# Kernel tuning notes

Hardware: AMD Instinct MI355X
Metric: run time of the kernel (lower is better)

The kernel has to match this reference:

```python
import jax, jax.numpy as jnp
import numpy as np

B, N, D0 = 128, 128, 512   # batch, n_objects, obj_dim
H, KD, R = 32, 64, 16      # n_heads, key_dim, n_relations
D = D0 + 1                 # with temporal tag

def setup_inputs() -> dict:
    key = jax.random.key(0)
    k1, k2, k3, k4, k5 = jax.random.split(key, 5)
    s = 0.02
    return {
        'obj_seq': jax.random.normal(k1, (B, N, D0), jnp.float32),
        'W_k':  jax.random.normal(k2, (KD, D), jnp.float32) * s,
        'W_q1': jax.random.normal(k3, (H * KD, D * N), jnp.float32) * s,
        'W_q2': jax.random.normal(k4, (H * KD, D * N), jnp.float32) * s,
        'W_s':  jax.random.normal(k5, (R, D), jnp.float32) * s,
    }

def reference(obj_seq, W_k, W_q1, W_q2, W_s):
    b, n, _ = obj_seq.shape
    # append temporal tag channel: obj -> [B, N, D]
    tag = jnp.broadcast_to(jnp.arange(n, dtype=obj_seq.dtype)[None, :, None], (b, n, 1))
    obj = jnp.concatenate([obj_seq, tag], axis=2)
    flat = obj.reshape(b, -1)                      # [B, N*D]
    Q1 = (flat @ W_q1.T).reshape(b, H, KD)         # [B, H, KD]
    Q2 = (flat @ W_q2.T).reshape(b, H, KD)
    K = obj @ W_k.T                                # [B, N, KD]
    # scores [B, N, H], softmax over objects (dim=1 in torch)
    A1 = jax.nn.softmax(jnp.einsum('bhk,bnk->bnh', Q1, K), axis=1)
    A2 = jax.nn.softmax(jnp.einsum('bhk,bnk->bnh', Q2, K), axis=1)
    # attention-weighted object sums: [B, H, D]
    E1 = jnp.einsum('bnh,bnd->bhd', A1, obj)
    E2 = jnp.einsum('bnh,bnd->bhd', A2, obj)
    Dr = E1 @ W_s.T - E2 @ W_s.T                   # [B, H, R]
    Dr = jnp.concatenate([Dr, E1[:, :, -1:], E2[:, :, -1:]], axis=2)  # [B, H, R+2]
    return Dr.reshape(b, -1)                       # [B, H*(R+2)]
```

## Files before the change

kernel.cpp:

```cpp
#include <hip/hip_runtime.h>
#include <cstdint>

typedef _Float16 f16;
typedef _Float16 f16x8 __attribute__((ext_vector_type(8)));
typedef short s16x8 __attribute__((ext_vector_type(8)));
typedef unsigned u32x4 __attribute__((ext_vector_type(4)));
typedef float f32x4 __attribute__((ext_vector_type(4)));
typedef float floatx4 __attribute__((ext_vector_type(4)));

#define KTOT 65664
#define KSTEPS 2052
#define DP 544

__device__ __forceinline__ void gload_lds16(const void* g, void* l) {
  __builtin_amdgcn_global_load_lds(
      (const __attribute__((address_space(1))) void*)g,
      (__attribute__((address_space(3))) void*)l, 16, 0, 0);
}

__device__ __forceinline__ unsigned bfpack(float e0, float e1) {
  return (__float_as_uint(e0) >> 16) | (__float_as_uint(e1) & 0xffff0000u);
}
__device__ __forceinline__ float bfhi(float x) {
  return __uint_as_float(__float_as_uint(x) & 0xffff0000u);
}

__global__ void prep_flat(const float* __restrict__ obj_seq, char* __restrict__ flatA) {
  int o = blockIdx.x * 256 + threadIdx.x;
  int row = o & 127;
  int k8 = (o >> 7) & 3;
  int pl = (o >> 9) & 1;
  int kb = o >> 10;
  int k0 = kb * 32 + k8 * 8;
  unsigned w[4];
#pragma unroll
  for (int j = 0; j < 8; j += 2) {
    float v[2];
#pragma unroll
    for (int jj = 0; jj < 2; ++jj) {
      int k = k0 + j + jj;
      int n = k / 513;
      int d = k - n * 513;
      float x = (d < 512) ? obj_seq[(((size_t)(row << 7) + n) << 9) + d] : (float)n;
      if (pl) x = x - bfhi(x);
      v[jj] = x;
    }
    w[j >> 1] = bfpack(v[0], v[1]);
  }
  *(u32x4*)(flatA + (size_t)o * 16) = (u32x4){w[0], w[1], w[2], w[3]};
}

__global__ void prep_obj(const float* __restrict__ obj_seq, f16* __restrict__ objHi,
                         f16* __restrict__ objLo, f16* __restrict__ objT16) {
  __shared__ f16 tile[32][132];
  int b = blockIdx.x / 17, c = blockIdx.x - 17 * (blockIdx.x / 17);
  int t = threadIdx.x;
  if (c < 16) {
#pragma unroll
    for (int i = 0; i < 16; ++i) {
      int e = t + i * 256;
      int n = e >> 5, dd = e & 31;
      float v = obj_seq[(((size_t)(b << 7) + n) << 9) + (c << 5) + dd];
      f16 h = (f16)v;
      objHi[((size_t)((b << 7) + n)) * DP + (c << 5) + dd] = h;
      objLo[((size_t)((b << 7) + n)) * DP + (c << 5) + dd] = (f16)(v - (float)h);
      tile[dd][n] = h;
    }
    __syncthreads();
#pragma unroll
    for (int i = 0; i < 16; ++i) {
      int e = t + i * 256;
      int dd = e >> 7, n = e & 127;
      objT16[(((size_t)b * DP + (c << 5) + dd) << 7) + n] = tile[dd][n];
    }
  } else {
#pragma unroll
    for (int i = 0; i < 16; ++i) {
      int e = t + i * 256;
      int n = e >> 5, dd = e & 31;
      f16 h = (dd == 0) ? (f16)(float)n : (f16)0.f;
      objHi[((size_t)((b << 7) + n)) * DP + 512 + dd] = h;
      objLo[((size_t)((b << 7) + n)) * DP + 512 + dd] = (f16)0.f;
    }
#pragma unroll
    for (int i = 0; i < 16; ++i) {
      int e = t + i * 256;
      int dd = e >> 7, n = e & 127;
      objT16[(((size_t)b * DP + 512 + dd) << 7) + n] = (dd == 0) ? (f16)(float)n : (f16)0.f;
    }
  }
}

__global__ void prep_wk(const float* __restrict__ W_k, f16* __restrict__ WkHi,
                        f16* __restrict__ WkLo) {
  int o = blockIdx.x * 256 + threadIdx.x;
  int kd = o / DP, d = o - kd * DP;
  float v = (d < 513) ? W_k[kd * 513 + d] * 1024.f : 0.f;
  f16 h = (f16)v;
  WkHi[o] = h;
  WkLo[o] = (f16)(v - (float)h);
}

__global__ __launch_bounds__(512, 2) void qgemm(const char* __restrict__ flatA,
                                                const float* __restrict__ Wq1,
                                                const float* __restrict__ Wq2,
                                                float* __restrict__ Qpart) {
  __shared__ __align__(16) char smem[163840];
  const int tid = threadIdx.x;
  const int lane = tid & 63;
  const int wave = tid >> 6;
  const int wm = wave >> 2, wn = wave & 3;
  const int l15 = lane & 15, lk = lane >> 4;
  const int ntile = blockIdx.x & 31;
  const int ksp = blockIdx.x >> 5;
  const int t0 = (KSTEPS * ksp) >> 3;
  const int nt = ((KSTEPS * (ksp + 1)) >> 3) - t0;
  const float* Wsrc = (ntile < 16) ? (Wq1 + (size_t)ntile * 128 * KTOT)
                                   : (Wq2 + (size_t)(ntile - 16) * 128 * KTOT);

  const char* asrc = flatA + (size_t)t0 * 16384 + tid * 16;
  const float* wsrc0;
  const float* wsrc1;
  {
    int c0 = (tid >> 3), c1 = 64 + (tid >> 3);
    wsrc0 = Wsrc + (size_t)c0 * KTOT + (size_t)t0 * 32 + (((tid & 7) ^ (c0 & 7)) << 2);
    wsrc1 = Wsrc + (size_t)c1 * KTOT + (size_t)t0 * 32 + (((tid & 7) ^ (c1 & 7)) << 2);
  }

  int aoff[2][4];
#pragma unroll
  for (int pl = 0; pl < 2; ++pl)
#pragma unroll
    for (int mi = 0; mi < 4; ++mi)
      aoff[pl][mi] = pl * 8192 + lk * 2048 + (wm * 64 + mi * 16 + l15) * 16;
  int woff[2][2];
#pragma unroll
  for (int nf = 0; nf < 2; ++nf) {
    int col = wn * 32 + nf * 16 + l15;
#pragma unroll
    for (int j = 0; j < 2; ++j)
      woff[nf][j] = col * 128 + (((2 * lk + j) ^ (col & 7)) << 4);
  }

  f32x4 acc[4][2];
#pragma unroll
  for (int mi = 0; mi < 4; ++mi)
#pragma unroll
    for (int nf = 0; nf < 2; ++nf) acc[mi][nf] = (f32x4){0.f, 0.f, 0.f, 0.f};

  auto stageA = [&](int tt, int slot) {
    char* S = smem + slot * 16384;
    gload_lds16(asrc + (size_t)tt * 16384, S + tid * 16);
    gload_lds16(asrc + (size_t)tt * 16384 + 8192, S + 8192 + tid * 16);
  };
  auto stageW = [&](int tt, int slot) {
    char* S = smem + 49152 + slot * 16384;
    gload_lds16(wsrc0 + (size_t)tt * 32, S + tid * 16);
    gload_lds16(wsrc1 + (size_t)tt * 32, S + 8192 + tid * 16);
  };

  auto compute = [&](const char* SA, const char* SW) {
    s16x8 wH[2], wL[2];
#pragma unroll
    for (int nf = 0; nf < 2; ++nf) {
      floatx4 a = *(const floatx4*)(SW + woff[nf][0]);
      floatx4 b = *(const floatx4*)(SW + woff[nf][1]);
      u32x4 H = (u32x4){bfpack(a[0], a[1]), bfpack(a[2], a[3]),
                        bfpack(b[0], b[1]), bfpack(b[2], b[3])};
      float l0 = a[0] - bfhi(a[0]), l1 = a[1] - bfhi(a[1]);
      float l2 = a[2] - bfhi(a[2]), l3 = a[3] - bfhi(a[3]);
      float l4 = b[0] - bfhi(b[0]), l5 = b[1] - bfhi(b[1]);
      float l6 = b[2] - bfhi(b[2]), l7 = b[3] - bfhi(b[7 - 7 + 3]);
      u32x4 L = (u32x4){bfpack(l0, l1), bfpack(l2, l3), bfpack(l4, l5), bfpack(l6, l7)};
      wH[nf] = *(s16x8*)&H;
      wL[nf] = *(s16x8*)&L;
    }
    __builtin_amdgcn_s_setprio(1);
#pragma unroll
    for (int mi = 0; mi < 4; ++mi) {
      s16x8 aH = *(const s16x8*)(SA + aoff[0][mi]);
      s16x8 aL = *(const s16x8*)(SA + aoff[1][mi]);
#pragma unroll
      for (int nf = 0; nf < 2; ++nf) {
        acc[mi][nf] = __builtin_amdgcn_mfma_f32_16x16x32_bf16(aH, wH[nf], acc[mi][nf], 0, 0, 0);
        acc[mi][nf] = __builtin_amdgcn_mfma_f32_16x16x32_bf16(aH, wL[nf], acc[mi][nf], 0, 0, 0);
        acc[mi][nf] = __builtin_amdgcn_mfma_f32_16x16x32_bf16(aL, wH[nf], acc[mi][nf], 0, 0, 0);
      }
    }
    __builtin_amdgcn_s_setprio(0);
  };

  stageW(0, 0); stageW(1, 1); stageW(2, 2); stageW(3, 3);
  stageA(0, 0);
  stageW(4, 4);
  stageA(1, 1);
  stageW(5, 5);

  int sa = 0, sw = 0, sa2 = 2, sw6 = 6;
  for (int t = 0; t < nt; ++t) {
    asm volatile("s_waitcnt vmcnt(6)" ::: "memory");
    __builtin_amdgcn_s_barrier();
    __builtin_amdgcn_sched_barrier(0);
    {
      int ta = t + 2; if (ta > nt - 1) ta = nt - 1;
      int tw = t + 6; if (tw > nt - 1) tw = nt - 1;
      stageA(ta, sa2);
      stageW(tw, sw6);
    }
    __builtin_amdgcn_sched_barrier(0);
    compute(smem + sa * 16384, smem + 49152 + sw * 16384);
    sa = (sa == 2) ? 0 : sa + 1;
    sa2 = (sa2 == 2) ? 0 : sa2 + 1;
    sw = (sw == 6) ? 0 : sw + 1;
    sw6 = (sw6 == 6) ? 0 : sw6 + 1;
  }
  asm volatile("s_waitcnt vmcnt(0)" ::: "memory");

  float* qout = Qpart + (size_t)ksp * 524288;
#pragma unroll
  for (int mi = 0; mi < 4; ++mi) {
    int row = wm * 64 + mi * 16 + lk * 4;
#pragma unroll
    for (int nf = 0; nf < 2; ++nf) {
      int col = ntile * 128 + wn * 32 + nf * 16 + l15;
#pragma unroll
      for (int j = 0; j < 4; ++j)
        qout[(size_t)(row + j) * 4096 + col] = acc[mi][nf][j];
    }
  }
}

__global__ __launch_bounds__(512, 1) void predinet_tail(
    const f16* __restrict__ objHi, const f16* __restrict__ objLo, const f16* __restrict__ objT16,
    const f16* __restrict__ WkHi, const f16* __restrict__ WkLo,
    const float* __restrict__ Qpart, const float* __restrict__ W_s, float* __restrict__ out) {
  __shared__ __align__(16) char smem[105984];
  const int b = blockIdx.x;
  const int tid = threadIdx.x, lane = tid & 63, wave = tid >> 6;
  const int l15 = lane & 15, lk = lane >> 4;

  f16* WT = (f16*)(smem);
  f16* Qh = (f16*)(smem + 17408);
  f16* Ql = (f16*)(smem + 26624);
  f16* Kh = (f16*)(smem + 35840);
  f16* Kl = (f16*)(smem + 54272);
  float* S = (float*)(smem + 72704);
  f16* E = (f16*)(smem + 17408);
  float* DL = (float*)(smem + 96832);

  {
    const float* qp = Qpart + (size_t)b * 4096 + tid * 8;
    floatx4 q0 = (floatx4){0.f, 0.f, 0.f, 0.f};
    floatx4 q1 = (floatx4){0.f, 0.f, 0.f, 0.f};
#pragma unroll
    for (int p = 0; p < 8; ++p) {
      q0 += *(const floatx4*)(qp + (size_t)p * 524288);
      q1 += *(const floatx4*)(qp + (size_t)p * 524288 + 4);
    }
    int hp = tid >> 3, kd = (tid * 8) & 63;
    f16x8 vh, vl;
#pragma unroll
    for (int j = 0; j < 4; ++j) {
      f16 h0 = (f16)q0[j]; vh[j] = h0; vl[j] = (f16)(q0[j] - (float)h0);
      f16 h1 = (f16)q1[j]; vh[4 + j] = h1; vl[4 + j] = (f16)(q1[j] - (float)h1);
    }
    *(f16x8*)(Qh + hp * 72 + kd) = vh;
    *(f16x8*)(Ql + hp * 72 + kd) = vl;
  }
  {
    f32x4 acc[4];
#pragma unroll
    for (int nf = 0; nf < 4; ++nf) acc[nf] = (f32x4){0.f, 0.f, 0.f, 0.f};
    const f16* arowH = objHi + ((size_t)(b * 128) + wave * 16 + l15) * DP + lk * 8;
    const f16* arowL = objLo + ((size_t)(b * 128) + wave * 16 + l15) * DP + lk * 8;
    const f16* bhi = WkHi + (size_t)l15 * DP + lk * 8;
    const f16* blo = WkLo + (size_t)l15 * DP + lk * 8;
    for (int ks = 0; ks < 17; ++ks) {
      f16x8 ah = *(const f16x8*)(arowH + ks * 32);
      f16x8 al = *(const f16x8*)(arowL + ks * 32);
#pragma unroll
      for (int nf = 0; nf < 4; ++nf) {
        f16x8 h = *(const f16x8*)(bhi + (size_t)nf * 16 * DP + ks * 32);
        f16x8 l = *(const f16x8*)(blo + (size_t)nf * 16 * DP + ks * 32);
        acc[nf] = __builtin_amdgcn_mfma_f32_16x16x32_f16(ah, h, acc[nf], 0, 0, 0);
        acc[nf] = __builtin_amdgcn_mfma_f32_16x16x32_f16(ah, l, acc[nf], 0, 0, 0);
        acc[nf] = __builtin_amdgcn_mfma_f32_16x16x32_f16(al, h, acc[nf], 0, 0, 0);
      }
    }
#pragma unroll
    for (int nf = 0; nf < 4; ++nf)
#pragma unroll
      for (int j = 0; j < 4; ++j) {
        float kv = acc[nf][j] * (1.f / 1024.f);
        f16 h = (f16)kv;
        Kh[(wave * 16 + lk * 4 + j) * 72 + nf * 16 + l15] = h;
        Kl[(wave * 16 + lk * 4 + j) * 72 + nf * 16 + l15] = (f16)(kv - (float)h);
      }
  }
  __syncthreads();
  {
    f32x4 acc[4];
#pragma unroll
    for (int nf = 0; nf < 4; ++nf) acc[nf] = (f32x4){0.f, 0.f, 0.f, 0.f};
#pragma unroll
    for (int ks = 0; ks < 2; ++ks) {
      f16x8 ah = *(const f16x8*)(Kh + (wave * 16 + l15) * 72 + ks * 32 + lk * 8);
      f16x8 al = *(const f16x8*)(Kl + (wave * 16 + l15) * 72 + ks * 32 + lk * 8);
#pragma unroll
      for (int nf = 0; nf < 4; ++nf) {
        f16x8 bh = *(const f16x8*)(Qh + (nf * 16 + l15) * 72 + ks * 32 + lk * 8);
        f16x8 bl = *(const f16x8*)(Ql + (nf * 16 + l15) * 72 + ks * 32 + lk * 8);
        acc[nf] = __builtin_amdgcn_mfma_f32_16x16x32_f16(ah, bh, acc[nf], 0, 0, 0);
        acc[nf] = __builtin_amdgcn_mfma_f32_16x16x32_f16(ah, bl, acc[nf], 0, 0, 0);
        acc[nf] = __builtin_amdgcn_mfma_f32_16x16x32_f16(al, bh, acc[nf], 0, 0, 0);
      }
    }
#pragma unroll
    for (int nf = 0; nf < 4; ++nf)
#pragma unroll
      for (int j = 0; j < 4; ++j)
        S[(wave * 16 + lk * 4 + j) * 65 + nf * 16 + l15] = acc[nf][j];
  }
  __syncthreads();
  {
#pragma unroll
    for (int ci = 0; ci < 8; ++ci) {
      int c = wave * 8 + ci;
      float s0 = S[lane * 65 + c], s1 = S[(lane + 64) * 65 + c];
      float m = fmaxf(s0, s1);
      for (int off = 32; off; off >>= 1) m = fmaxf(m, __shfl_xor(m, off));
      float e0 = __expf(s0 - m), e1 = __expf(s1 - m);
      float sum = e0 + e1;
      for (int off = 32; off; off >>= 1) sum += __shfl_xor(sum, off);
      float inv = 1.f / sum;
      WT[c * 136 + lane] = (f16)(e0 * inv);
      WT[c * 136 + 64 + lane] = (f16)(e1 * inv);
    }
  }
  __syncthreads();
  {
    f16x8 bw[4][4];
#pragma unroll
    for (int nf = 0; nf < 4; ++nf)
#pragma unroll
      for (int ks = 0; ks < 4; ++ks)
        bw[nf][ks] = *(const f16x8*)(WT + (nf * 16 + l15) * 136 + ks * 32 + lk * 8);
    for (int r = 0; r < 5; ++r) {
      int mi = r * 8 + wave;
      if (mi >= 34) break;
      const f16* arow = objT16 + (((size_t)b * DP + mi * 16 + l15) << 7) + lk * 8;
      f16x8 a[4];
#pragma unroll
      for (int ks = 0; ks < 4; ++ks) a[ks] = *(const f16x8*)(arow + ks * 32);
#pragma unroll
      for (int nf = 0; nf < 4; ++nf) {
        f32x4 acc = (f32x4){0.f, 0.f, 0.f, 0.f};
#pragma unroll
        for (int ks = 0; ks < 4; ++ks)
          acc = __builtin_amdgcn_mfma_f32_16x16x32_f16(a[ks], bw[nf][ks], acc, 0, 0, 0);
#pragma unroll
        for (int j = 0; j < 4; ++j)
          E[(mi * 16 + lk * 4 + j) * 73 + nf * 16 + l15] = (f16)acc[j];
      }
    }
  }
  __syncthreads();
  {
    f16* Ws16 = WT;
    for (int i = tid; i < 16 * DP; i += 512) {
      int r = i / DP, d = i - r * DP;
      Ws16[i] = (f16)((d < 513) ? W_s[r * 513 + d] : 0.f);
    }
  }
  __syncthreads();
  if (wave < 4) {
    const f16* Ws16 = WT;
    f32x4 acc = (f32x4){0.f, 0.f, 0.f, 0.f};
    for (int ks = 0; ks < 17; ++ks) {
      f16x8 a = *(const f16x8*)(Ws16 + l15 * DP + ks * 32 + lk * 8);
      f16x8 bv;
#pragma unroll
      for (int jj = 0; jj < 8; ++jj)
        bv[jj] = E[(ks * 32 + lk * 8 + jj) * 73 + wave * 16 + l15];
      acc = __builtin_amdgcn_mfma_f32_16x16x32_f16(a, bv, acc, 0, 0, 0);
    }
#pragma unroll
    for (int j = 0; j < 4; ++j) DL[(lk * 4 + j) * 64 + wave * 16 + l15] = acc[j];
  }
  __syncthreads();
  {
    int h = tid >> 4, r = tid & 15;
    float v = DL[r * 64 + h] - DL[r * 64 + 32 + h];
    out[(size_t)b * 576 + h * 18 + r] = v;
    if (tid < 64) {
      int set = tid >> 5, hh = tid & 31;
      out[(size_t)b * 576 + hh * 18 + 16 + set] = (float)E[512 * 73 + set * 32 + hh];
    }
  }
}

extern "C" void kernel_launch(void* const* d_in, const int* in_sizes, int n_in,
                              void* d_out, int out_size, void* d_ws, size_t ws_size,
                              hipStream_t stream) {
  const float* obj_seq = (const float*)d_in[0];
  const float* W_k = (const float*)d_in[1];
  const float* W_q1 = (const float*)d_in[2];
  const float* W_q2 = (const float*)d_in[3];
  const float* W_s = (const float*)d_in[4];
  float* out = (float*)d_out;

  char* ws = (char*)d_ws;
  size_t off = 0;
  auto carve = [&](size_t bytes) -> char* {
    char* p = ws + off;
    off += (bytes + 255) & ~(size_t)255;
    return p;
  };
  char* flatA = carve((size_t)KSTEPS * 16384);
  f16* objHi = (f16*)carve((size_t)16384 * DP * 2);
  f16* objLo = (f16*)carve((size_t)16384 * DP * 2);
  f16* objT16 = (f16*)carve((size_t)128 * DP * 128 * 2);
  f16* WkHi = (f16*)carve((size_t)64 * DP * 2);
  f16* WkLo = (f16*)carve((size_t)64 * DP * 2);
  float* Qpart = (float*)carve((size_t)8 * 524288 * 4);
  (void)ws_size; (void)in_sizes; (void)n_in; (void)out_size;

  prep_flat<<<8208, 256, 0, stream>>>(obj_seq, flatA);
  prep_obj<<<2176, 256, 0, stream>>>(obj_seq, objHi, objLo, objT16);
  prep_wk<<<136, 256, 0, stream>>>(W_k, WkHi, WkLo);
  qgemm<<<256, 512, 0, stream>>>(flatA, W_q1, W_q2, Qpart);
  predinet_tail<<<128, 512, 0, stream>>>(objHi, objLo, objT16, WkHi, WkLo, Qpart, W_s, out);
}
```

Before: 367.7 us.

## Unify A/W staging into a 5-slot pipeline and reorder block-to-tile mapping

```diff
diff --git a/kernel.cpp b/kernel.cpp
--- a/kernel.cpp
+++ b/kernel.cpp
@@ -111,8 +111,8 @@
   const int wave = tid >> 6;
   const int wm = wave >> 2, wn = wave & 3;
   const int l15 = lane & 15, lk = lane >> 4;
-  const int ntile = blockIdx.x & 31;
-  const int ksp = blockIdx.x >> 5;
+  const int ksp = blockIdx.x & 7;
+  const int ntile = blockIdx.x >> 3;
   const int t0 = (KSTEPS * ksp) >> 3;
   const int nt = ((KSTEPS * (ksp + 1)) >> 3) - t0;
   const float* Wsrc = (ntile < 16) ? (Wq1 + (size_t)ntile * 128 * KTOT)
@@ -148,15 +148,13 @@
 #pragma unroll
     for (int nf = 0; nf < 2; ++nf) acc[mi][nf] = (f32x4){0.f, 0.f, 0.f, 0.f};
 
-  auto stageA = [&](int tt, int slot) {
-    char* S = smem + slot * 16384;
-    gload_lds16(asrc + (size_t)tt * 16384, S + tid * 16);
-    gload_lds16(asrc + (size_t)tt * 16384 + 8192, S + 8192 + tid * 16);
-  };
-  auto stageW = [&](int tt, int slot) {
-    char* S = smem + 49152 + slot * 16384;
-    gload_lds16(wsrc0 + (size_t)tt * 32, S + tid * 16);
-    gload_lds16(wsrc1 + (size_t)tt * 32, S + 8192 + tid * 16);
+  auto stage = [&](int tt, int slot) {
+    char* SA = smem + slot * 16384;
+    char* SW = smem + 81920 + slot * 16384;
+    gload_lds16(asrc + (size_t)tt * 16384, SA + tid * 16);
+    gload_lds16(asrc + (size_t)tt * 16384 + 8192, SA + 8192 + tid * 16);
+    gload_lds16(wsrc0 + (size_t)tt * 32, SW + tid * 16);
+    gload_lds16(wsrc1 + (size_t)tt * 32, SW + 8192 + tid * 16);
   };
 
   auto compute = [&](const char* SA, const char* SW) {
@@ -170,7 +168,7 @@
       float l0 = a[0] - bfhi(a[0]), l1 = a[1] - bfhi(a[1]);
       float l2 = a[2] - bfhi(a[2]), l3 = a[3] - bfhi(a[3]);
       float l4 = b[0] - bfhi(b[0]), l5 = b[1] - bfhi(b[1]);
-      float l6 = b[2] - bfhi(b[2]), l7 = b[3] - bfhi(b[7 - 7 + 3]);
+      float l6 = b[2] - bfhi(b[2]), l7 = b[3] - bfhi(b[3]);
       u32x4 L = (u32x4){bfpack(l0, l1), bfpack(l2, l3), bfpack(l4, l5), bfpack(l6, l7)};
       wH[nf] = *(s16x8*)&H;
       wL[nf] = *(s16x8*)&L;
@@ -190,29 +188,19 @@
     __builtin_amdgcn_s_setprio(0);
   };
 
-  stageW(0, 0); stageW(1, 1); stageW(2, 2); stageW(3, 3);
-  stageA(0, 0);
-  stageW(4, 4);
-  stageA(1, 1);
-  stageW(5, 5);
-
-  int sa = 0, sw = 0, sa2 = 2, sw6 = 6;
+  stage(0, 0); stage(1, 1); stage(2, 2); stage(3, 3);
+
+  int sl = 0, s4 = 4;
   for (int t = 0; t < nt; ++t) {
-    asm volatile("s_waitcnt vmcnt(6)" ::: "memory");
+    asm volatile("s_waitcnt vmcnt(12)" ::: "memory");
     __builtin_amdgcn_s_barrier();
     __builtin_amdgcn_sched_barrier(0);
-    {
-      int ta = t + 2; if (ta > nt - 1) ta = nt - 1;
-      int tw = t + 6; if (tw > nt - 1) tw = nt - 1;
-      stageA(ta, sa2);
-      stageW(tw, sw6);
-    }
+    int t4 = t + 4; if (t4 > nt - 1) t4 = nt - 1;
+    stage(t4, s4);
     __builtin_amdgcn_sched_barrier(0);
-    compute(smem + sa * 16384, smem + 49152 + sw * 16384);
-    sa = (sa == 2) ? 0 : sa + 1;
-    sa2 = (sa2 == 2) ? 0 : sa2 + 1;
-    sw = (sw == 6) ? 0 : sw + 1;
-    sw6 = (sw6 == 6) ? 0 : sw6 + 1;
+    compute(smem + sl * 16384, smem + 81920 + sl * 16384);
+    sl = (sl == 4) ? 0 : sl + 1;
+    s4 = (s4 == 4) ? 0 : s4 + 1;
   }
   asm volatile("s_waitcnt vmcnt(0)" ::: "memory");
 
```

Result: no change. 364.5 us (-0.9%).
